# Optimization experiments

Hardware: AMD Instinct MI355X
Metric: run time of the kernel (lower is better)

The kernel has to match this reference:

```python
import jax, jax.numpy as jnp
import numpy as np

B, F_, T, H, K = 4, 128, 32000, 64, 32  # batch, feat(=input_channel), time, hidden_channel, kernel_size
G = 3 * F_  # GRU gate width (r,z,n)


def setup_inputs() -> dict:
    key = jax.random.key(0)
    ks = jax.random.split(key, 12)
    s = 1.0 / np.sqrt(F_)  # torch GRU init scale
    u = lambda k, sh: jax.random.uniform(k, sh, jnp.float32, -s, s)
    return {
        "x": jax.random.normal(ks[0], (B, F_, T), jnp.float32),
        "kernel": jax.random.uniform(ks[1], (H, 1, K), jnp.float32),
        "kernel_weight": jax.random.uniform(ks[2], (H, 1, K), jnp.float32),
        "prelu_a": jnp.float32(0.25),
        "W_ih_f": u(ks[3], (G, F_)), "W_hh_f": u(ks[4], (G, F_)),
        "b_ih_f": u(ks[5], (G,)), "b_hh_f": u(ks[6], (G,)),
        "W_ih_b": u(ks[7], (G, F_)), "W_hh_b": u(ks[8], (G, F_)),
        "b_ih_b": u(ks[9], (G,)), "b_hh_b": u(ks[10], (G,)),
    }


def _gru_dir(x, Wih, Whh, bih, bhh):
    # x: [B, T, I]; torch GRU gate order is (r, z, n)
    X = jnp.einsum('bti,gi->btg', x, Wih) + bih  # precompute input projections [B,T,3H]
    X = jnp.moveaxis(X, 1, 0)                    # [T,B,3H]
    Hh = Whh.shape[1]

    def step(h, xt):
        g = h @ Whh.T + bhh
        xr, xz, xn = jnp.split(xt, 3, axis=-1)
        gr, gz, gn = jnp.split(g, 3, axis=-1)
        r = jax.nn.sigmoid(xr + gr)
        z = jax.nn.sigmoid(xz + gz)
        n = jnp.tanh(xn + r * gn)
        h = (1.0 - z) * n + z * h
        return h, h

    h0 = jnp.zeros((x.shape[0], Hh), x.dtype)
    _, hs = jax.lax.scan(step, h0, X)  # [T,B,H]
    return jnp.moveaxis(hs, 0, 1)      # [B,T,H]


def reference(x, kernel, kernel_weight, prelu_a,
              W_ih_f, W_hh_f, b_ih_f, b_hh_f,
              W_ih_b, W_hh_b, b_ih_b, b_hh_b):
    Bb, Ff, Tt = x.shape
    # conv1d(flip(x_pad), k).flip() summed over the H filters is a causal FIR
    # filter; sum_h conv(x, k_h) == conv(x, sum_h k_h), so collapse the bank first.
    keff = (kernel * kernel_weight).sum(axis=0).reshape(-1)  # [K]
    xp = jnp.pad(x.reshape(Bb * Ff, 1, Tt), ((0, 0), (0, 0), (K - 1, 0)))
    rhs = keff[::-1].reshape(1, 1, K)  # correlate with reversed kernel == true convolution
    out = jax.lax.conv_general_dilated(
        xp, rhs, window_strides=(1,), padding='VALID',
        dimension_numbers=('NCH', 'OIH', 'NCH')).reshape(Bb, Ff, Tt)
    out = jnp.where(out >= 0, out, prelu_a * out)  # PReLU (single shared slope)

    seq = jnp.swapaxes(out, 1, 2)  # [B,T,F]
    hf = _gru_dir(seq, W_ih_f, W_hh_f, b_ih_f, b_hh_f)
    hb = _gru_dir(seq[:, ::-1], W_ih_b, W_hh_b, b_ih_b, b_hh_b)[:, ::-1]
    # concat(fwd,bwd) on channel dim then sum halves == fwd + bwd
    return jnp.swapaxes(hf + hb, 1, 2)  # [B,F,T]
```

## Files before the change

### kernel.cpp

```cpp
#include <hip/hip_runtime.h>
#include <hip/hip_fp16.h>

#define B_ 4
#define F__ 128
#define T_ 32000
#define K_ 32
#define G_ 384

#define CHUNK_L2 64
#define NCHUNK   (T_ / CHUNK_L2)
#define WARM2    640
#define NSTEPS   (WARM2 + CHUNK_L2)
#define BLKS_PER_DIR ((B_ * NCHUNK) / 16)

typedef _Float16 half8 __attribute__((ext_vector_type(8)));
typedef _Float16 half4 __attribute__((ext_vector_type(4)));
typedef float float4v __attribute__((ext_vector_type(4)));
typedef unsigned int uint32;

#define WS_KEFF    0u
#define WS_XBIAS   4096u
#define WS_BHHN    8192u
#define WS_WHHPK   16384u
#define WS_WIHHI   212992u
#define WS_WIHLO   409600u
#define WS_SEQ     1048576u
#define WS_SEQL    (WS_SEQ + 32768000u)
#define WS_X       66584576u

__device__ __forceinline__ void block_sync_lds() {
    asm volatile("s_waitcnt lgkmcnt(0)" ::: "memory");
    __builtin_amdgcn_s_barrier();
    asm volatile("" ::: "memory");
}

__global__ void prep_kernel(const float* __restrict__ kern, const float* __restrict__ kw,
                            const float* __restrict__ Wihf, const float* __restrict__ Whhf,
                            const float* __restrict__ bihf, const float* __restrict__ bhhf,
                            const float* __restrict__ Wihb, const float* __restrict__ Whhb,
                            const float* __restrict__ bihb, const float* __restrict__ bhhb,
                            char* __restrict__ ws) {
    const float SRZ = -1.442695041f, SN = -2.885390082f;
    float*    keff  = (float*)(ws + WS_KEFF);
    float*    xbias = (float*)(ws + WS_XBIAS);
    float*    bhhn  = (float*)(ws + WS_BHHN);
    _Float16* whhpk = (_Float16*)(ws + WS_WHHPK);
    _Float16* wihhi = (_Float16*)(ws + WS_WIHHI);
    _Float16* wihlo = (_Float16*)(ws + WS_WIHLO);
    int tid = threadIdx.x;

    if (tid < 32) {
        float s = 0.f;
        for (int h = 0; h < 64; h++) s += kern[h * 32 + tid] * kw[h * 32 + tid];
        keff[tid] = s;
    }
    for (int g = tid; g < 768; g += 256) {
        int dir = g / 384, gl = g % 384;
        const float* bih = dir ? bihb : bihf;
        const float* bhh = dir ? bhhb : bhhf;
        float sc = (gl < 256) ? SRZ : SN;
        xbias[g] = sc * (bih[gl] + (gl < 256 ? bhh[gl] : 0.f));
    }
    for (int i = tid; i < 256; i += 256) {
        int dir = i >> 7, j = i & 127;
        bhhn[i] = SN * (dir ? bhhb : bhhf)[256 + j];
    }
    for (int i = tid; i < 2 * 384 * 128; i += 256) {
        int dir = i / (384 * 128), rem = i % (384 * 128);
        int gl = rem / 128;
        float sc = (gl < 256) ? SRZ : SN;
        whhpk[i] = (_Float16)(sc * (dir ? Whhb : Whhf)[rem]);
        float w = sc * (dir ? Wihb : Wihf)[rem];
        _Float16 hi = (_Float16)w;
        wihhi[i] = hi;
        wihlo[i] = (_Float16)(w - (float)hi);
    }
}

__global__ __launch_bounds__(256) void fir_kernel(const float* __restrict__ x,
                                                  const float* __restrict__ prelu_a,
                                                  char* __restrict__ ws) {
    __shared__ float kefs[32];
    __shared__ float tilef[32 * 66];
    const float* keff = (const float*)(ws + WS_KEFF);
    _Float16* seqh = (_Float16*)(ws + WS_SEQ);
    _Float16* seql = (_Float16*)(ws + WS_SEQL);
    int tid = threadIdx.x;
    if (tid < 32) kefs[tid] = keff[tid];
    __syncthreads();

    int b = blockIdx.z, f0 = blockIdx.y * 32, t0 = blockIdx.x * 64;
    int tl = tid & 63, fl = tid >> 6;
    float a = prelu_a[0];
    int t = t0 + tl;
    for (int ff = fl; ff < 32; ff += 4) {
        const float* xr = x + (((size_t)b * F__ + f0 + ff) * T_ + t);
        float s = 0.f;
#pragma unroll
        for (int k = 0; k < 32; k++) {
            if (k <= t) s += kefs[k] * xr[-k];
        }
        tilef[ff * 66 + tl] = s >= 0.f ? s : a * s;
    }
    __syncthreads();
#pragma unroll
    for (int pass = 0; pass < 8; pass++) {
        int idx = pass * 256 + tid;
        int f2 = idx & 31, t2 = idx >> 5;
        float v = tilef[f2 * 66 + t2];
        _Float16 hi = (_Float16)v;
        _Float16 lo = (_Float16)(v - (float)hi);
        size_t o = ((size_t)b * T_ + t0 + t2) * 128 + f0 + f2;
        seqh[o] = hi;
        seql[o] = lo;
    }
}

__global__ __launch_bounds__(256) void xproj_kernel(const char* __restrict__ ws) {
    const char* seqh = (const char*)(ws + WS_SEQ);
    const char* seql = (const char*)(ws + WS_SEQL);
    const _Float16* whi = (const _Float16*)(ws + WS_WIHHI);
    const _Float16* wlo = (const _Float16*)(ws + WS_WIHLO);
    const float*  xbias = (const float*)(ws + WS_XBIAS);
    _Float16* X = (_Float16*)(ws + WS_X);

    __shared__ char As[65536] __attribute__((aligned(16)));

    int tid = threadIdx.x;
    int wave = tid >> 6, lane = tid & 63;
    int n = lane & 15, quad = lane >> 4;
    int m0 = blockIdx.x * 128;

    {
        const char* gh = seqh + (size_t)m0 * 256;
        const char* gl2 = seql + (size_t)m0 * 256;
#pragma unroll
        for (int p = 0; p < 8; p++) {
            int s = p * 256 + tid;
            int row = s >> 4, c = s & 15;
            int gc = c ^ (row & 7);
            int go = row * 256 + gc * 16;
            *(uint4*)(As + s * 16) = *(const uint4*)(gh + go);
            *(uint4*)(As + 32768 + s * 16) = *(const uint4*)(gl2 + go);
        }
    }
    __syncthreads();

    int rdA[4];
#pragma unroll
    for (int kt = 0; kt < 4; kt++)
        rdA[kt] = n * 256 + (((kt * 4 + quad) ^ (n & 7)) * 16);

#pragma unroll 1
    for (int g = 0; g < 12; g++) {
        int gcol = g * 64 + wave * 16 + n;
        half8 bh[4], bl[4];
#pragma unroll
        for (int k = 0; k < 4; k++) {
            bh[k] = *(const half8*)(whi + (size_t)gcol * 128 + k * 32 + quad * 8);
            bl[k] = *(const half8*)(wlo + (size_t)gcol * 128 + k * 32 + quad * 8);
        }
        float bias = xbias[gcol];
        int dirg = gcol / 384, gl3 = gcol - dirg * 384, gate = gl3 >> 7, fq = gl3 & 127;
        int xcol = dirg * 384 + (gate < 2 ? (fq * 2 + gate) : (256 + fq));

#pragma unroll 1
        for (int i = 0; i < 8; i++) {
            float4v acc = {0.f, 0.f, 0.f, 0.f};
#pragma unroll
            for (int k = 0; k < 4; k++) {
                half8 ah = *(const half8*)(As + rdA[k] + i * 4096);
                half8 al = *(const half8*)(As + 32768 + rdA[k] + i * 4096);
                acc = __builtin_amdgcn_mfma_f32_16x16x32_f16(ah, bh[k], acc, 0, 0, 0);
                acc = __builtin_amdgcn_mfma_f32_16x16x32_f16(al, bh[k], acc, 0, 0, 0);
                acc = __builtin_amdgcn_mfma_f32_16x16x32_f16(ah, bl[k], acc, 0, 0, 0);
            }
            int rbase = m0 + i * 16 + quad * 4;
#pragma unroll
            for (int r = 0; r < 4; r++)
                X[(size_t)(rbase + r) * 768 + xcol] = (_Float16)(acc[r] + bias);
        }
    }
}

__global__ __launch_bounds__(512) void gru_kernel(const char* __restrict__ ws) {
    int dir = blockIdx.y;
    int blk = blockIdx.x;
    int tid = threadIdx.x;
    int wave = tid >> 6, lane = tid & 63;
    int n = lane & 15, quad = lane >> 4;
    int f0 = wave * 16 + quad * 4;
    int fw = wave * 16 + n;
    int b4 = n & 3;
    int chunk = blk * 4 + (n >> 2);
    int ts0 = chunk * CHUNK_L2 - WARM2;

    const _Float16* whh = (const _Float16*)(ws + WS_WHHPK) + (size_t)dir * 384 * 128;
    const float*    bhn = (const float*)(ws + WS_BHHN);
    half8 wr[4], wz[4], wn[4];
#pragma unroll
    for (int kt = 0; kt < 4; kt++) {
        wr[kt] = *(const half8*)(whh + (size_t)fw * 128 + kt * 32 + quad * 8);
        wz[kt] = *(const half8*)(whh + (size_t)(fw + 128) * 128 + kt * 32 + quad * 8);
        wn[kt] = *(const half8*)(whh + (size_t)(fw + 256) * 128 + kt * 32 + quad * 8);
    }
    float bnv[4];
#pragma unroll
    for (int reg = 0; reg < 4; reg++) bnv[reg] = bhn[dir * 128 + f0 + reg];

    const char* px = (const char*)(ws + WS_X) + dir * 768 + (size_t)b4 * T_ * 1536;
    const int xstep = dir ? -1536 : 1536;
    const uint32 colrz = (uint32)f0 * 4u;
    const uint32 coln  = 512u + (uint32)f0 * 2u;

    _Float16* dsto = (_Float16*)(ws + (dir ? WS_SEQL : WS_SEQ)) + (size_t)b4 * T_ * 128;

    __shared__ _Float16 hbuf[2][2048] __attribute__((aligned(16)));
    for (int i = tid; i < 2048; i += 512) hbuf[0][i] = (_Float16)0.f;

    const int rdoff = lane * 8;
    const int wroff = (wave >> 1) * 512 + ((2 * wave + (quad >> 1)) & 3) * 128
                      + n * 8 + (quad & 1) * 4;

    float h0 = 0.f, h1 = 0.f, h2 = 0.f, h3 = 0.f;

    auto rowof = [&](int t) -> uint32 {
        int c = t < 0 ? 0 : (t > T_ - 1 ? T_ - 1 : t);
        return (uint32)(dir ? (T_ - 1 - c) : c);
    };

    half8 rzA, rzB;
    half4 xnA, xnB;
    {
        uint32 o0 = rowof(ts0) * 1536u, o1 = rowof(ts0 + 1) * 1536u;
        rzA = *(const half8*)(px + o0 + colrz);
        xnA = *(const half4*)(px + o0 + coln);
        rzB = *(const half8*)(px + o1 + colrz);
        xnB = *(const half4*)(px + o1 + coln);
    }
    uint32 orz = rowof(ts0 + 2) * 1536u + colrz;
    uint32 on  = rowof(ts0 + 2) * 1536u + coln;
    int tpf = ts0 + 2;
    int tc  = ts0;

    auto body = [&](half8& rz, half4& xn, int r) {
        float4v ar, az, an;
#pragma unroll
        for (int reg = 0; reg < 4; reg++) {
            ar[reg] = (float)rz[2 * reg];
            az[reg] = (float)rz[2 * reg + 1];
            an[reg] = bnv[reg];
        }
        float xnv[4];
#pragma unroll
        for (int reg = 0; reg < 4; reg++) xnv[reg] = (float)xn[reg];
        rz = *(const half8*)(px + orz);
        xn = *(const half4*)(px + on);
        if ((uint32)tpf < (uint32)(T_ - 1)) { orz += xstep; on += xstep; }
        ++tpf;

        block_sync_lds();
        const _Float16* hs = &hbuf[r & 1][rdoff];
        half8 ha[4];
#pragma unroll
        for (int kt = 0; kt < 4; kt++)
            ha[kt] = *(const half8*)(hs + kt * 512);

#pragma unroll
        for (int kt = 0; kt < 4; kt++) {
            ar = __builtin_amdgcn_mfma_f32_16x16x32_f16(wr[kt], ha[kt], ar, 0, 0, 0);
            az = __builtin_amdgcn_mfma_f32_16x16x32_f16(wz[kt], ha[kt], az, 0, 0, 0);
            an = __builtin_amdgcn_mfma_f32_16x16x32_f16(wn[kt], ha[kt], an, 0, 0, 0);
        }
        bool neg = tc < 0;
#define GATE(reg, hvar)                                                       \
        {                                                                     \
            float rg = __builtin_amdgcn_rcpf(1.f + __builtin_amdgcn_exp2f(ar[reg])); \
            float zg = __builtin_amdgcn_rcpf(1.f + __builtin_amdgcn_exp2f(az[reg])); \
            float tt = __builtin_amdgcn_rcpf(1.f + __builtin_amdgcn_exp2f(xnv[reg] + rg * an[reg])); \
            float ng = 2.f * tt - 1.f;                                        \
            hvar = ng + zg * (hvar - ng);                                     \
            if (neg) hvar = 0.f;                                              \
        }
        GATE(0, h0)
        GATE(1, h1)
        GATE(2, h2)
        GATE(3, h3)
#undef GATE
        half4 hv = {(_Float16)h0, (_Float16)h1, (_Float16)h2, (_Float16)h3};
        *(half4*)(&hbuf[(r + 1) & 1][wroff]) = hv;
        if (r >= WARM2) {
            int tout = dir ? (T_ - 1 - tc) : tc;
            __builtin_nontemporal_store(hv, (half4*)(dsto + (size_t)tout * 128 + f0));
        }
        ++tc;
    };

#pragma unroll 1
    for (int r = 0; r < NSTEPS; r += 2) {
        body(rzA, xnA, r);
        body(rzB, xnB, r + 1);
    }
}

__global__ __launch_bounds__(256) void merge_kernel(const char* __restrict__ ws,
                                                    float* __restrict__ out) {
    __shared__ float tile[64 * 65];
    const _Float16* fh = (const _Float16*)(ws + WS_SEQ);
    const _Float16* bw = (const _Float16*)(ws + WS_SEQL);
    int b = blockIdx.z, f0 = blockIdx.y * 64, t0 = blockIdx.x * 64;
    int tid = threadIdx.x;
    int cl = tid & 63, rw = tid >> 6;
#pragma unroll
    for (int p = 0; p < 16; p++) {
        int t = t0 + p * 4 + rw;
        size_t o = ((size_t)b * T_ + t) * 128 + f0 + cl;
        tile[cl * 65 + p * 4 + rw] = (float)fh[o] + (float)bw[o];
    }
    __syncthreads();
#pragma unroll
    for (int p = 0; p < 16; p++) {
        int fo = f0 + p * 4 + rw;
        __builtin_nontemporal_store(tile[(p * 4 + rw) * 65 + cl],
                                    out + ((size_t)b * F__ + fo) * T_ + t0 + cl);
    }
}

extern "C" void kernel_launch(void* const* d_in, const int* in_sizes, int n_in,
                              void* d_out, int out_size, void* d_ws, size_t ws_size,
                              hipStream_t stream) {
    (void)in_sizes; (void)n_in; (void)ws_size; (void)out_size;
    const float* x    = (const float*)d_in[0];
    const float* kern = (const float*)d_in[1];
    const float* kw   = (const float*)d_in[2];
    const float* pa   = (const float*)d_in[3];
    const float* Wihf = (const float*)d_in[4];
    const float* Whhf = (const float*)d_in[5];
    const float* bihf = (const float*)d_in[6];
    const float* bhhf = (const float*)d_in[7];
    const float* Wihb = (const float*)d_in[8];
    const float* Whhb = (const float*)d_in[9];
    const float* bihb = (const float*)d_in[10];
    const float* bhhb = (const float*)d_in[11];
    float* out = (float*)d_out;
    char* ws = (char*)d_ws;

    prep_kernel<<<1, 256, 0, stream>>>(kern, kw, Wihf, Whhf, bihf, bhhf,
                                       Wihb, Whhb, bihb, bhhb, ws);

    fir_kernel<<<dim3(T_ / 64, F__ / 32, B_), 256, 0, stream>>>(x, pa, ws);

    xproj_kernel<<<dim3((B_ * T_) / 128), 256, 0, stream>>>(ws);

    gru_kernel<<<dim3(BLKS_PER_DIR, 2), 512, 0, stream>>>(ws);

    merge_kernel<<<dim3(T_ / 64, F__ / 64, B_), 256, 0, stream>>>(ws, out);
}
```

Before: 1.027 ms.

## Split xproj gate columns across three blocks and hoist weight fragments into registers

```diff
diff --git a/kernel.cpp b/kernel.cpp
--- a/kernel.cpp
+++ b/kernel.cpp
@@ -116,7 +116,7 @@
     }
 }
 
-__global__ __launch_bounds__(256) void xproj_kernel(const char* __restrict__ ws) {
+__global__ __launch_bounds__(256, 2) void xproj_kernel(const char* __restrict__ ws) {
     const char* seqh = (const char*)(ws + WS_SEQ);
     const char* seql = (const char*)(ws + WS_SEQL);
     const _Float16* whi = (const _Float16*)(ws + WS_WIHHI);
@@ -129,7 +129,24 @@
     int tid = threadIdx.x;
     int wave = tid >> 6, lane = tid & 63;
     int n = lane & 15, quad = lane >> 4;
-    int m0 = blockIdx.x * 128;
+    int tile = blockIdx.x / 3, pass = blockIdx.x % 3;
+    int m0 = tile * 128;
+
+    half8 bh[4][4], bl[4][4];
+    float bias[4];
+    int xcol[4];
+#pragma unroll
+    for (int g = 0; g < 4; g++) {
+        int gcol = (pass * 4 + g) * 64 + wave * 16 + n;
+#pragma unroll
+        for (int k = 0; k < 4; k++) {
+            bh[g][k] = *(const half8*)(whi + (size_t)gcol * 128 + k * 32 + quad * 8);
+            bl[g][k] = *(const half8*)(wlo + (size_t)gcol * 128 + k * 32 + quad * 8);
+        }
+        bias[g] = xbias[gcol];
+        int dirg = gcol / 384, gl3 = gcol - dirg * 384, gate = gl3 >> 7, fq = gl3 & 127;
+        xcol[g] = dirg * 384 + (gate < 2 ? (fq * 2 + gate) : (256 + fq));
+    }
 
     {
         const char* gh = seqh + (size_t)m0 * 256;
@@ -152,33 +169,26 @@
         rdA[kt] = n * 256 + (((kt * 4 + quad) ^ (n & 7)) * 16);
 
 #pragma unroll 1
-    for (int g = 0; g < 12; g++) {
-        int gcol = g * 64 + wave * 16 + n;
-        half8 bh[4], bl[4];
+    for (int i = 0; i < 8; i++) {
+        half8 ah[4], al[4];
 #pragma unroll
         for (int k = 0; k < 4; k++) {
-            bh[k] = *(const half8*)(whi + (size_t)gcol * 128 + k * 32 + quad * 8);
-            bl[k] = *(const half8*)(wlo + (size_t)gcol * 128 + k * 32 + quad * 8);
-        }
-        float bias = xbias[gcol];
-        int dirg = gcol / 384, gl3 = gcol - dirg * 384, gate = gl3 >> 7, fq = gl3 & 127;
-        int xcol = dirg * 384 + (gate < 2 ? (fq * 2 + gate) : (256 + fq));
-
-#pragma unroll 1
-        for (int i = 0; i < 8; i++) {
+            ah[k] = *(const half8*)(As + rdA[k] + i * 4096);
+            al[k] = *(const half8*)(As + 32768 + rdA[k] + i * 4096);
+        }
+        int rbase = m0 + i * 16 + quad * 4;
+#pragma unroll
+        for (int g = 0; g < 4; g++) {
             float4v acc = {0.f, 0.f, 0.f, 0.f};
 #pragma unroll
             for (int k = 0; k < 4; k++) {
-                half8 ah = *(const half8*)(As + rdA[k] + i * 4096);
-                half8 al = *(const half8*)(As + 32768 + rdA[k] + i * 4096);
-                acc = __builtin_amdgcn_mfma_f32_16x16x32_f16(ah, bh[k], acc, 0, 0, 0);
-                acc = __builtin_amdgcn_mfma_f32_16x16x32_f16(al, bh[k], acc, 0, 0, 0);
-                acc = __builtin_amdgcn_mfma_f32_16x16x32_f16(ah, bl[k], acc, 0, 0, 0);
+                acc = __builtin_amdgcn_mfma_f32_16x16x32_f16(ah[k], bh[g][k], acc, 0, 0, 0);
+                acc = __builtin_amdgcn_mfma_f32_16x16x32_f16(al[k], bh[g][k], acc, 0, 0, 0);
+                acc = __builtin_amdgcn_mfma_f32_16x16x32_f16(ah[k], bl[g][k], acc, 0, 0, 0);
             }
-            int rbase = m0 + i * 16 + quad * 4;
 #pragma unroll
             for (int r = 0; r < 4; r++)
-                X[(size_t)(rbase + r) * 768 + xcol] = (_Float16)(acc[r] + bias);
+                X[(size_t)(rbase + r) * 768 + xcol[g]] = (_Float16)(acc[r] + bias[g]);
         }
     }
 }
@@ -350,7 +360,7 @@
 
     fir_kernel<<<dim3(T_ / 64, F__ / 32, B_), 256, 0, stream>>>(x, pa, ws);
 
-    xproj_kernel<<<dim3((B_ * T_) / 128), 256, 0, stream>>>(ws);
+    xproj_kernel<<<dim3(3 * (B_ * T_) / 128), 256, 0, stream>>>(ws);
 
     gru_kernel<<<dim3(BLKS_PER_DIR, 2), 512, 0, stream>>>(ws);
 
```

After: 1.032 ms. No clear change (+0.6%).
